# Kernel tuning notes

Hardware: AMD Instinct MI355X
Metric: run time of the kernel (lower is better)

The kernel has to match this reference:

```python
import jax, jax.numpy as jnp
import numpy as np

B, C, T, H, NCLS = 512, 22, 1000, 64, 4


def setup_inputs() -> dict:
    key = jax.random.key(0)
    ks = jax.random.split(key, 8)
    s_ih = 1.0 / np.sqrt(H)
    x = jax.random.normal(ks[0], (B, C, T), dtype=jnp.float32)
    # PyTorch LSTM params: gate order [i, f, g, o], each of size H
    W_ih = jax.random.uniform(ks[1], (4 * H, C), minval=-s_ih, maxval=s_ih, dtype=jnp.float32)
    W_hh = jax.random.uniform(ks[2], (4 * H, H), minval=-s_ih, maxval=s_ih, dtype=jnp.float32)
    b_ih = jax.random.uniform(ks[3], (4 * H,), minval=-s_ih, maxval=s_ih, dtype=jnp.float32)
    b_hh = jax.random.uniform(ks[4], (4 * H,), minval=-s_ih, maxval=s_ih, dtype=jnp.float32)
    s_fc = 1.0 / np.sqrt(H * T)
    W_fc = jax.random.uniform(ks[5], (NCLS, H * T), minval=-s_fc, maxval=s_fc, dtype=jnp.float32)
    b_fc = jax.random.uniform(ks[6], (NCLS,), minval=-s_fc, maxval=s_fc, dtype=jnp.float32)
    return {"x": x, "W_ih": W_ih, "W_hh": W_hh, "b_ih": b_ih, "b_hh": b_hh,
            "W_fc": W_fc, "b_fc": b_fc}


def _lstm(xs, W_ih, W_hh, b_ih, b_hh):
    # xs: [B, T, C] -> outputs [B, T, H]
    b = xs.shape[0]
    # precompute input projections for all timesteps: [T, B, 4H]
    x_proj = jnp.einsum('btc,gc->tbg', xs, W_ih) + (b_ih + b_hh)
    h0 = jnp.zeros((b, W_hh.shape[1]), xs.dtype)
    c0 = jnp.zeros_like(h0)

    def step(carry, xp):
        h, c = carry
        gates = xp + h @ W_hh.T  # [B, 4H]
        i, f, g, o = jnp.split(gates, 4, axis=-1)
        i = jax.nn.sigmoid(i)
        f = jax.nn.sigmoid(f)
        g = jnp.tanh(g)
        o = jax.nn.sigmoid(o)
        c = f * c + i * g
        h = o * jnp.tanh(c)
        return (h, c), h

    _, hs = jax.lax.scan(step, (h0, c0), x_proj)  # hs: [T, B, H]
    return jnp.transpose(hs, (1, 0, 2))  # [B, T, H]


def reference(x, W_ih, W_hh, b_ih, b_hh, W_fc, b_fc):
    xs = jnp.transpose(x, (0, 2, 1))  # [B, T, C]  (permute(0,2,1))
    hs = _lstm(xs, W_ih, W_hh, b_ih, b_hh)  # [B, T, H]
    flat = hs.reshape(hs.shape[0], -1)  # [B, T*H], time-major per row
    logits = flat @ W_fc.T + b_fc  # [B, 4]
    return jax.nn.softmax(logits, axis=1)
```

## Files before the change

kernel.cpp:

```cpp
#include <hip/hip_runtime.h>

#define BB   512
#define CC   22
#define TT   1000
#define HH   64
#define NCLS 4
#define TC   250
#define NCHUNK (TT / TC)
#define XROW 12

typedef _Float16 f16;
typedef __attribute__((ext_vector_type(2))) _Float16 h2;

__device__ __forceinline__ float sigm(float x) {
    return 1.0f / (1.0f + __expf(-x));
}
__device__ __forceinline__ float tanh_(float x) {
    float e = __expf(-2.0f * fabsf(x));
    float r = (1.0f - e) / (1.0f + e);
    return copysignf(r, x);
}

__device__ __forceinline__ h2 u2h(unsigned u) {
    union { unsigned u; h2 h; } c; c.u = u; return c.h;
}
__device__ __forceinline__ unsigned h2u(h2 h) {
    union { unsigned u; h2 h; } c; c.h = h; return c.u;
}

__global__ __launch_bounds__(64, 1) void lstm_wave(
    const float* __restrict__ x,
    const float* __restrict__ W_ih,
    const float* __restrict__ W_hh,
    const float* __restrict__ b_ih,
    const float* __restrict__ b_hh,
    const float* __restrict__ W_fc,
    const float* __restrict__ b_fc,
    float* __restrict__ out)
{
    __shared__ __align__(16) h2  xs[TC][XROW];
    __shared__ __align__(16) f16 hbuf[HH];

    const int lane = threadIdx.x;
    const int r    = blockIdx.x;

    unsigned whh[4][32];
    unsigned wih[4][11];
    float bias[4];
    #pragma unroll
    for (int g = 0; g < 4; ++g) {
        const int row = g * HH + lane;
        const float* wr = W_hh + row * HH;
        #pragma unroll
        for (int k = 0; k < 32; ++k)
            whh[g][k] = h2u(h2{(f16)wr[2 * k], (f16)wr[2 * k + 1]});
        const float* wi = W_ih + row * CC;
        #pragma unroll
        for (int k = 0; k < 11; ++k)
            wih[g][k] = h2u(h2{(f16)wi[2 * k], (f16)wi[2 * k + 1]});
        bias[g] = b_ih[row] + b_hh[row];
    }
    #pragma unroll
    for (int g = 0; g < 4; ++g) {
        #pragma unroll
        for (int k = 0; k < 32; ++k) asm volatile("" : "+v"(whh[g][k]));
        #pragma unroll
        for (int k = 0; k < 11; ++k) asm volatile("" : "+v"(wih[g][k]));
        asm volatile("" : "+v"(bias[g]));
    }

    hbuf[lane] = (f16)0.0f;
    float c = 0.0f;
    float fc0 = 0.f, fc1 = 0.f, fc2 = 0.f, fc3 = 0.f;
    const float* p0 = W_fc + 0 * (TT * HH) + lane;
    const float* p1 = W_fc + 1 * (TT * HH) + lane;
    const float* p2 = W_fc + 2 * (TT * HH) + lane;
    const float* p3 = W_fc + 3 * (TT * HH) + lane;
    const float* xrow = x + (size_t)r * (CC * TT);

    for (int chunk = 0; chunk < NCHUNK; ++chunk) {
        for (int tb = 0; tb < TC; tb += 64) {
            const int t = tb + lane;
            if (t < TC) {
                const float* gx = xrow + chunk * TC + t;
                union { h2 h[XROW]; uint4 q[3]; } U;
                #pragma unroll
                for (int k = 0; k < 11; ++k)
                    U.h[k] = h2{(f16)gx[(2 * k) * TT], (f16)gx[(2 * k + 1) * TT]};
                U.h[11] = h2{(f16)0.0f, (f16)0.0f};
                uint4* dst = (uint4*)&xs[t][0];
                dst[0] = U.q[0]; dst[1] = U.q[1]; dst[2] = U.q[2];
            }
        }

        for (int tt = 0; tt < TC; ++tt) {
            union { uint4 q[8]; h2 h[32]; } H;
            const uint4* hr = (const uint4*)hbuf;
            #pragma unroll
            for (int i = 0; i < 8; ++i) H.q[i] = hr[i];

            union { uint4 q[3]; h2 h[XROW]; } X;
            const uint4* xr = (const uint4*)&xs[tt][0];
            X.q[0] = xr[0]; X.q[1] = xr[1]; X.q[2] = xr[2];

            float w0 = *p0, w1 = *p1, w2 = *p2, w3 = *p3;
            p0 += HH; p1 += HH; p2 += HH; p3 += HH;

            float a0 = bias[0], a1 = bias[1], a2 = bias[2], a3 = bias[3];
            #pragma unroll
            for (int k = 0; k < 11; ++k) {
                a0 = __builtin_amdgcn_fdot2(X.h[k], u2h(wih[0][k]), a0, false);
                a1 = __builtin_amdgcn_fdot2(X.h[k], u2h(wih[1][k]), a1, false);
                a2 = __builtin_amdgcn_fdot2(X.h[k], u2h(wih[2][k]), a2, false);
                a3 = __builtin_amdgcn_fdot2(X.h[k], u2h(wih[3][k]), a3, false);
            }
            #pragma unroll
            for (int k = 0; k < 32; ++k) {
                a0 = __builtin_amdgcn_fdot2(H.h[k], u2h(whh[0][k]), a0, false);
                a1 = __builtin_amdgcn_fdot2(H.h[k], u2h(whh[1][k]), a1, false);
                a2 = __builtin_amdgcn_fdot2(H.h[k], u2h(whh[2][k]), a2, false);
                a3 = __builtin_amdgcn_fdot2(H.h[k], u2h(whh[3][k]), a3, false);
            }

            float iv = sigm(a0), fv = sigm(a1), gv = tanh_(a2), ov = sigm(a3);
            c = fv * c + iv * gv;
            float h = ov * tanh_(c);

            fc0 += h * w0; fc1 += h * w1; fc2 += h * w2; fc3 += h * w3;

            hbuf[lane] = (f16)h;
        }
    }

    #pragma unroll
    for (int off = 32; off; off >>= 1) {
        fc0 += __shfl_down(fc0, off);
        fc1 += __shfl_down(fc1, off);
        fc2 += __shfl_down(fc2, off);
        fc3 += __shfl_down(fc3, off);
    }
    if (lane == 0) {
        float l0 = fc0 + b_fc[0], l1 = fc1 + b_fc[1];
        float l2 = fc2 + b_fc[2], l3 = fc3 + b_fc[3];
        float m  = fmaxf(fmaxf(l0, l1), fmaxf(l2, l3));
        float e0 = __expf(l0 - m), e1 = __expf(l1 - m);
        float e2 = __expf(l2 - m), e3 = __expf(l3 - m);
        float s  = e0 + e1 + e2 + e3;
        float4 o; o.x = e0 / s; o.y = e1 / s; o.z = e2 / s; o.w = e3 / s;
        *(float4*)(out + r * NCLS) = o;
    }
}

extern "C" void kernel_launch(void* const* d_in, const int* in_sizes, int n_in,
                              void* d_out, int out_size, void* d_ws, size_t ws_size,
                              hipStream_t stream) {
    const float* x    = (const float*)d_in[0];
    const float* W_ih = (const float*)d_in[1];
    const float* W_hh = (const float*)d_in[2];
    const float* b_ih = (const float*)d_in[3];
    const float* b_hh = (const float*)d_in[4];
    const float* W_fc = (const float*)d_in[5];
    const float* b_fc = (const float*)d_in[6];
    float* out = (float*)d_out;

    lstm_wave<<<BB, 64, 0, stream>>>(x, W_ih, W_hh, b_ih, b_hh, W_fc, b_fc, out);
}
```

Measured before the change: 681.1 us.

## Precompute input projections per chunk with MFMA and defer FC accumulation

The input projection (W_ih·x) moves out of the serial recurrence. For each 64-step chunk it is computed with 16x16x32 f16 MFMA instructions and stored as packed f16 gate preactivations in shared memory. Hidden states of a chunk are kept in LDS, and the FC dot products run after the chunk, so the W_fc loads leave the critical serial path. Divisions are replaced by hardware reciprocals. The cost is extra LDS use, f16 rounding of the projected inputs, and W_ih fragments reloaded from global memory every chunk.

Result: slower. 1.281 ms (+88.1%).

```diff
diff --git a/kernel.cpp b/kernel.cpp
--- a/kernel.cpp
+++ b/kernel.cpp
@@ -5,30 +5,40 @@
 #define TT   1000
 #define HH   64
 #define NCLS 4
-#define TC   250
-#define NCHUNK (TT / TC)
-#define XROW 12
+#define FCW  (TT * HH)
+#define CH   64
+#define NCH  16
+#define XPS  528
 
 typedef _Float16 f16;
 typedef __attribute__((ext_vector_type(2))) _Float16 h2;
+typedef __attribute__((ext_vector_type(8))) _Float16 f16x8;
+typedef __attribute__((ext_vector_type(4))) float    f32x4;
+
+union U16x8 { uint4 q; f16x8 h; f16 e[8]; };
 
 __device__ __forceinline__ float sigm(float x) {
-    return 1.0f / (1.0f + __expf(-x));
+    float e = __expf(-x);
+    return __builtin_amdgcn_rcpf(1.0f + e);
 }
 __device__ __forceinline__ float tanh_(float x) {
     float e = __expf(-2.0f * fabsf(x));
-    float r = (1.0f - e) / (1.0f + e);
+    float r = (1.0f - e) * __builtin_amdgcn_rcpf(1.0f + e);
     return copysignf(r, x);
 }
-
 __device__ __forceinline__ h2 u2h(unsigned u) {
     union { unsigned u; h2 h; } c; c.u = u; return c.h;
 }
 __device__ __forceinline__ unsigned h2u(h2 h) {
     union { unsigned u; h2 h; } c; c.h = h; return c.u;
 }
-
-__global__ __launch_bounds__(64, 1) void lstm_wave(
+__device__ __forceinline__ unsigned pack2(float a, float b) {
+    union { unsigned u; h2 h; } c;
+    c.h = h2{(f16)a, (f16)b};
+    return c.u;
+}
+
+__global__ __launch_bounds__(64, 1) void lstm_fused(
     const float* __restrict__ x,
     const float* __restrict__ W_ih,
     const float* __restrict__ W_hh,
@@ -38,14 +48,16 @@
     const float* __restrict__ b_fc,
     float* __restrict__ out)
 {
-    __shared__ __align__(16) h2  xs[TC][XROW];
-    __shared__ __align__(16) f16 hbuf[HH];
+    __shared__ __align__(16) f16  xs[CH][32];
+    __shared__ __align__(16) char xpb[CH * XPS];
+    __shared__ __align__(16) f16  hst[CH][HH];
 
     const int lane = threadIdx.x;
     const int r    = blockIdx.x;
+    const int q    = lane >> 4;
+    const int c    = lane & 15;
 
     unsigned whh[4][32];
-    unsigned wih[4][11];
     float bias[4];
     #pragma unroll
     for (int g = 0; g < 4; ++g) {
@@ -53,82 +65,129 @@
         const float* wr = W_hh + row * HH;
         #pragma unroll
         for (int k = 0; k < 32; ++k)
-            whh[g][k] = h2u(h2{(f16)wr[2 * k], (f16)wr[2 * k + 1]});
-        const float* wi = W_ih + row * CC;
-        #pragma unroll
-        for (int k = 0; k < 11; ++k)
-            wih[g][k] = h2u(h2{(f16)wi[2 * k], (f16)wi[2 * k + 1]});
+            whh[g][k] = pack2(wr[2 * k], wr[2 * k + 1]);
         bias[g] = b_ih[row] + b_hh[row];
     }
     #pragma unroll
     for (int g = 0; g < 4; ++g) {
         #pragma unroll
         for (int k = 0; k < 32; ++k) asm volatile("" : "+v"(whh[g][k]));
-        #pragma unroll
-        for (int k = 0; k < 11; ++k) asm volatile("" : "+v"(wih[g][k]));
         asm volatile("" : "+v"(bias[g]));
     }
 
-    hbuf[lane] = (f16)0.0f;
-    float c = 0.0f;
+    hst[CH - 1][lane] = (f16)0.0f;
+    float cst = 0.0f;
     float fc0 = 0.f, fc1 = 0.f, fc2 = 0.f, fc3 = 0.f;
-    const float* p0 = W_fc + 0 * (TT * HH) + lane;
-    const float* p1 = W_fc + 1 * (TT * HH) + lane;
-    const float* p2 = W_fc + 2 * (TT * HH) + lane;
-    const float* p3 = W_fc + 3 * (TT * HH) + lane;
     const float* xrow = x + (size_t)r * (CC * TT);
 
-    for (int chunk = 0; chunk < NCHUNK; ++chunk) {
-        for (int tb = 0; tb < TC; tb += 64) {
-            const int t = tb + lane;
-            if (t < TC) {
-                const float* gx = xrow + chunk * TC + t;
-                union { h2 h[XROW]; uint4 q[3]; } U;
+    for (int ch = 0; ch < NCH; ++ch) {
+        const int T0 = ch * CH;
+        const int Lc = (T0 + CH <= TT) ? CH : (TT - T0);
+
+        {
+            const int t = lane;
+            union { h2 h[16]; uint4 qq[4]; } U;
+            if (t < Lc) {
+                const float* gx = xrow + T0 + t;
                 #pragma unroll
                 for (int k = 0; k < 11; ++k)
                     U.h[k] = h2{(f16)gx[(2 * k) * TT], (f16)gx[(2 * k + 1) * TT]};
-                U.h[11] = h2{(f16)0.0f, (f16)0.0f};
-                uint4* dst = (uint4*)&xs[t][0];
-                dst[0] = U.q[0]; dst[1] = U.q[1]; dst[2] = U.q[2];
-            }
-        }
-
-        for (int tt = 0; tt < TC; ++tt) {
-            union { uint4 q[8]; h2 h[32]; } H;
-            const uint4* hr = (const uint4*)hbuf;
+                #pragma unroll
+                for (int k = 11; k < 16; ++k) U.h[k] = h2{(f16)0.0f, (f16)0.0f};
+            } else {
+                #pragma unroll
+                for (int k = 0; k < 16; ++k) U.h[k] = h2{(f16)0.0f, (f16)0.0f};
+            }
+            uint4* dst = (uint4*)&xs[t][0];
+            dst[0] = U.qq[0]; dst[1] = U.qq[1]; dst[2] = U.qq[2]; dst[3] = U.qq[3];
+        }
+
+        #pragma unroll
+        for (int mt = 0; mt < 4; ++mt) {
+            f16x8 Afr[4];
             #pragma unroll
-            for (int i = 0; i < 8; ++i) H.q[i] = hr[i];
-
-            union { uint4 q[3]; h2 h[XROW]; } X;
-            const uint4* xr = (const uint4*)&xs[tt][0];
-            X.q[0] = xr[0]; X.q[1] = xr[1]; X.q[2] = xr[2];
-
-            float w0 = *p0, w1 = *p1, w2 = *p2, w3 = *p3;
-            p0 += HH; p1 += HH; p2 += HH; p3 += HH;
-
-            float a0 = bias[0], a1 = bias[1], a2 = bias[2], a3 = bias[3];
+            for (int g = 0; g < 4; ++g) {
+                const float* wbase = W_ih + (size_t)(g * HH + 16 * mt + c) * CC;
+                U16x8 u;
+                #pragma unroll
+                for (int e = 0; e < 8; ++e) {
+                    const int chn = 8 * q + e;
+                    u.e[e] = (f16)(chn < CC ? wbase[chn] : 0.0f);
+                }
+                Afr[g] = u.h;
+            }
             #pragma unroll
-            for (int k = 0; k < 11; ++k) {
-                a0 = __builtin_amdgcn_fdot2(X.h[k], u2h(wih[0][k]), a0, false);
-                a1 = __builtin_amdgcn_fdot2(X.h[k], u2h(wih[1][k]), a1, false);
-                a2 = __builtin_amdgcn_fdot2(X.h[k], u2h(wih[2][k]), a2, false);
-                a3 = __builtin_amdgcn_fdot2(X.h[k], u2h(wih[3][k]), a3, false);
-            }
-            #pragma unroll
-            for (int k = 0; k < 32; ++k) {
-                a0 = __builtin_amdgcn_fdot2(H.h[k], u2h(whh[0][k]), a0, false);
-                a1 = __builtin_amdgcn_fdot2(H.h[k], u2h(whh[1][k]), a1, false);
-                a2 = __builtin_amdgcn_fdot2(H.h[k], u2h(whh[2][k]), a2, false);
-                a3 = __builtin_amdgcn_fdot2(H.h[k], u2h(whh[3][k]), a3, false);
-            }
-
-            float iv = sigm(a0), fv = sigm(a1), gv = tanh_(a2), ov = sigm(a3);
-            c = fv * c + iv * gv;
-            float h = ov * tanh_(c);
-
-            fc0 += h * w0; fc1 += h * w1; fc2 += h * w2; fc3 += h * w3;
-
-            hbuf[lane] = (f16)h;
+            for (int tg = 0; tg < 4; ++tg) {
+                U16x8 Bf;
+                Bf.q = *(const uint4*)&xs[16 * tg + c][8 * q];
+                const f32x4 z = {0.f, 0.f, 0.f, 0.f};
+                f32x4 Di = __builtin_amdgcn_mfma_f32_16x16x32_f16(Afr[0], Bf.h, z, 0, 0, 0);
+                f32x4 Df = __builtin_amdgcn_mfma_f32_16x16x32_f16(Afr[1], Bf.h, z, 0, 0, 0);
+                f32x4 Dg = __builtin_amdgcn_mfma_f32_16x16x32_f16(Afr[2], Bf.h, z, 0, 0, 0);
+                f32x4 Do = __builtin_amdgcn_mfma_f32_16x16x32_f16(Afr[3], Bf.h, z, 0, 0, 0);
+                char* wp = xpb + (size_t)(16 * tg + c) * XPS + (16 * mt + 4 * q) * 8;
+                #pragma unroll
+                for (int rr = 0; rr < 4; ++rr) {
+                    uint2 v;
+                    v.x = pack2(Di[rr], Df[rr]);
+                    v.y = pack2(Dg[rr], Do[rr]);
+                    *(uint2*)(wp + rr * 8) = v;
+                }
+            }
+        }
+
+        for (int tt = 0; tt < Lc; ++tt) {
+            const int pr = (tt == 0) ? (CH - 1) : tt - 1;
+
+            const uint2 xv = *(const uint2*)(xpb + (size_t)tt * XPS + lane * 8);
+            const h2 pif = u2h(xv.x), pgo = u2h(xv.y);
+            float a0 = bias[0] + (float)pif[0];
+            float a1 = bias[1] + (float)pif[1];
+            float a2 = bias[2] + (float)pgo[0];
+            float a3 = bias[3] + (float)pgo[1];
+
+            const uint4* hr = (const uint4*)&hst[pr][0];
+            {
+                union { uint4 qq[4]; h2 h[16]; } H;
+                H.qq[0] = hr[0]; H.qq[1] = hr[1]; H.qq[2] = hr[2]; H.qq[3] = hr[3];
+                #pragma unroll
+                for (int k = 0; k < 16; ++k) {
+                    a0 = __builtin_amdgcn_fdot2(H.h[k], u2h(whh[0][k]), a0, false);
+                    a1 = __builtin_amdgcn_fdot2(H.h[k], u2h(whh[1][k]), a1, false);
+                    a2 = __builtin_amdgcn_fdot2(H.h[k], u2h(whh[2][k]), a2, false);
+                    a3 = __builtin_amdgcn_fdot2(H.h[k], u2h(whh[3][k]), a3, false);
+                }
+            }
+            {
+                union { uint4 qq[4]; h2 h[16]; } H;
+                H.qq[0] = hr[4]; H.qq[1] = hr[5]; H.qq[2] = hr[6]; H.qq[3] = hr[7];
+                #pragma unroll
+                for (int k = 0; k < 16; ++k) {
+                    a0 = __builtin_amdgcn_fdot2(H.h[k], u2h(whh[0][16 + k]), a0, false);
+                    a1 = __builtin_amdgcn_fdot2(H.h[k], u2h(whh[1][16 + k]), a1, false);
+                    a2 = __builtin_amdgcn_fdot2(H.h[k], u2h(whh[2][16 + k]), a2, false);
+                    a3 = __builtin_amdgcn_fdot2(H.h[k], u2h(whh[3][16 + k]), a3, false);
+                }
+            }
+
+            const float iv = sigm(a0), fv = sigm(a1);
+            const float gv = tanh_(a2), ov = sigm(a3);
+            cst = fv * cst + iv * gv;
+            const float h = ov * tanh_(cst);
+
+            hst[tt][lane] = (f16)h;
+        }
+
+        const float* w0 = W_fc + 0 * FCW + (size_t)T0 * HH + lane;
+        const float* w1 = W_fc + 1 * FCW + (size_t)T0 * HH + lane;
+        const float* w2 = W_fc + 2 * FCW + (size_t)T0 * HH + lane;
+        const float* w3 = W_fc + 3 * FCW + (size_t)T0 * HH + lane;
+        for (int tt = 0; tt < Lc; ++tt) {
+            const float hv = (float)hst[tt][lane];
+            fc0 += hv * w0[(size_t)tt * HH];
+            fc1 += hv * w1[(size_t)tt * HH];
+            fc2 += hv * w2[(size_t)tt * HH];
+            fc3 += hv * w3[(size_t)tt * HH];
         }
     }
 
@@ -140,13 +199,13 @@
         fc3 += __shfl_down(fc3, off);
     }
     if (lane == 0) {
-        float l0 = fc0 + b_fc[0], l1 = fc1 + b_fc[1];
-        float l2 = fc2 + b_fc[2], l3 = fc3 + b_fc[3];
-        float m  = fmaxf(fmaxf(l0, l1), fmaxf(l2, l3));
-        float e0 = __expf(l0 - m), e1 = __expf(l1 - m);
-        float e2 = __expf(l2 - m), e3 = __expf(l3 - m);
-        float s  = e0 + e1 + e2 + e3;
-        float4 o; o.x = e0 / s; o.y = e1 / s; o.z = e2 / s; o.w = e3 / s;
+        const float l0 = fc0 + b_fc[0], l1 = fc1 + b_fc[1];
+        const float l2 = fc2 + b_fc[2], l3 = fc3 + b_fc[3];
+        const float m  = fmaxf(fmaxf(l0, l1), fmaxf(l2, l3));
+        const float e0 = __expf(l0 - m), e1 = __expf(l1 - m);
+        const float e2 = __expf(l2 - m), e3 = __expf(l3 - m);
+        const float is = __builtin_amdgcn_rcpf(e0 + e1 + e2 + e3);
+        float4 o; o.x = e0 * is; o.y = e1 * is; o.z = e2 * is; o.w = e3 * is;
         *(float4*)(out + r * NCLS) = o;
     }
 }
@@ -163,5 +222,5 @@
     const float* b_fc = (const float*)d_in[6];
     float* out = (float*)d_out;
 
-    lstm_wave<<<BB, 64, 0, stream>>>(x, W_ih, W_hh, b_ih, b_hh, W_fc, b_fc, out);
-}
+    lstm_fused<<<BB, 64, 0, stream>>>(x, W_ih, W_hh, b_ih, b_hh, W_fc, b_fc, out);
+}
```

## Prefetch next-step input projection and defer FC accumulation to per-chunk pass

Applied to the files above, without the earlier changes.

Computes the input-projection dot products for timestep t+1 inside step t so they overlap the recurrent dot, shortening the serial dependency chain. Hidden states for each chunk are buffered in shared memory and the FC weights are consumed in a separate unrolled pass, removing global loads from the recurrence loop. Divisions in the activations and softmax are replaced with hardware reciprocal. This costs more shared memory and uses slightly less precise rcp math.

Measured after the change: 599.6 us. -12.0%, faster.

```diff
diff --git a/kernel.cpp b/kernel.cpp
--- a/kernel.cpp
+++ b/kernel.cpp
@@ -5,22 +5,22 @@
 #define TT   1000
 #define HH   64
 #define NCLS 4
-#define TC   250
-#define NCHUNK (TT / TC)
+#define FCW  (TT * HH)
+#define TCF  250
 #define XROW 12
 
 typedef _Float16 f16;
 typedef __attribute__((ext_vector_type(2))) _Float16 h2;
 
 __device__ __forceinline__ float sigm(float x) {
-    return 1.0f / (1.0f + __expf(-x));
+    float e = __expf(-x);
+    return __builtin_amdgcn_rcpf(1.0f + e);
 }
 __device__ __forceinline__ float tanh_(float x) {
     float e = __expf(-2.0f * fabsf(x));
-    float r = (1.0f - e) / (1.0f + e);
+    float r = (1.0f - e) * __builtin_amdgcn_rcpf(1.0f + e);
     return copysignf(r, x);
 }
-
 __device__ __forceinline__ h2 u2h(unsigned u) {
     union { unsigned u; h2 h; } c; c.u = u; return c.h;
 }
@@ -28,7 +28,21 @@
     union { unsigned u; h2 h; } c; c.h = h; return c.u;
 }
 
-__global__ __launch_bounds__(64, 1) void lstm_wave(
+#define XP_COMPUTE(TROW, O0, O1, O2, O3) do {                                  \
+    union { uint4 q[3]; h2 h[XROW]; } Xu_;                                     \
+    const uint4* xr_ = (const uint4*)&xs[(TROW)][0];                           \
+    Xu_.q[0] = xr_[0]; Xu_.q[1] = xr_[1]; Xu_.q[2] = xr_[2];                   \
+    O0 = bias[0]; O1 = bias[1]; O2 = bias[2]; O3 = bias[3];                    \
+    _Pragma("unroll")                                                          \
+    for (int k_ = 0; k_ < 11; ++k_) {                                          \
+        O0 = __builtin_amdgcn_fdot2(Xu_.h[k_], u2h(wih[0][k_]), O0, false);    \
+        O1 = __builtin_amdgcn_fdot2(Xu_.h[k_], u2h(wih[1][k_]), O1, false);    \
+        O2 = __builtin_amdgcn_fdot2(Xu_.h[k_], u2h(wih[2][k_]), O2, false);    \
+        O3 = __builtin_amdgcn_fdot2(Xu_.h[k_], u2h(wih[3][k_]), O3, false);    \
+    }                                                                          \
+} while (0)
+
+__global__ __launch_bounds__(64, 1) void lstm_one(
     const float* __restrict__ x,
     const float* __restrict__ W_ih,
     const float* __restrict__ W_hh,
@@ -38,15 +52,15 @@
     const float* __restrict__ b_fc,
     float* __restrict__ out)
 {
-    __shared__ __align__(16) h2  xs[TC][XROW];
-    __shared__ __align__(16) f16 hbuf[HH];
+    __shared__ __align__(16) h2  xs[TCF][XROW];
+    __shared__ __align__(16) f16 hst[TCF][HH];
 
     const int lane = threadIdx.x;
     const int r    = blockIdx.x;
 
     unsigned whh[4][32];
     unsigned wih[4][11];
-    float bias[4];
+    float    bias[4];
     #pragma unroll
     for (int g = 0; g < 4; ++g) {
         const int row = g * HH + lane;
@@ -69,20 +83,18 @@
         asm volatile("" : "+v"(bias[g]));
     }
 
-    hbuf[lane] = (f16)0.0f;
+    hst[TCF - 1][lane] = (f16)0.0f;
     float c = 0.0f;
     float fc0 = 0.f, fc1 = 0.f, fc2 = 0.f, fc3 = 0.f;
-    const float* p0 = W_fc + 0 * (TT * HH) + lane;
-    const float* p1 = W_fc + 1 * (TT * HH) + lane;
-    const float* p2 = W_fc + 2 * (TT * HH) + lane;
-    const float* p3 = W_fc + 3 * (TT * HH) + lane;
     const float* xrow = x + (size_t)r * (CC * TT);
 
-    for (int chunk = 0; chunk < NCHUNK; ++chunk) {
-        for (int tb = 0; tb < TC; tb += 64) {
+    for (int chunk = 0; chunk < 4; ++chunk) {
+        const int T0 = chunk * TCF;
+
+        for (int tb = 0; tb < TCF; tb += 64) {
             const int t = tb + lane;
-            if (t < TC) {
-                const float* gx = xrow + chunk * TC + t;
+            if (t < TCF) {
+                const float* gx = xrow + T0 + t;
                 union { h2 h[XROW]; uint4 q[3]; } U;
                 #pragma unroll
                 for (int k = 0; k < 11; ++k)
@@ -93,27 +105,25 @@
             }
         }
 
-        for (int tt = 0; tt < TC; ++tt) {
+        float xpc0, xpc1, xpc2, xpc3;
+        XP_COMPUTE(0, xpc0, xpc1, xpc2, xpc3);
+
+        for (int tt = 0; tt < TCF; ++tt) {
+            const int pr = (tt == 0) ? TCF - 1 : tt - 1;
+
             union { uint4 q[8]; h2 h[32]; } H;
-            const uint4* hr = (const uint4*)hbuf;
+            const uint4* hr = (const uint4*)&hst[pr][0];
             #pragma unroll
             for (int i = 0; i < 8; ++i) H.q[i] = hr[i];
 
-            union { uint4 q[3]; h2 h[XROW]; } X;
-            const uint4* xr = (const uint4*)&xs[tt][0];
-            X.q[0] = xr[0]; X.q[1] = xr[1]; X.q[2] = xr[2];
-
-            float w0 = *p0, w1 = *p1, w2 = *p2, w3 = *p3;
-            p0 += HH; p1 += HH; p2 += HH; p3 += HH;
-
-            float a0 = bias[0], a1 = bias[1], a2 = bias[2], a3 = bias[3];
-            #pragma unroll
-            for (int k = 0; k < 11; ++k) {
-                a0 = __builtin_amdgcn_fdot2(X.h[k], u2h(wih[0][k]), a0, false);
-                a1 = __builtin_amdgcn_fdot2(X.h[k], u2h(wih[1][k]), a1, false);
-                a2 = __builtin_amdgcn_fdot2(X.h[k], u2h(wih[2][k]), a2, false);
-                a3 = __builtin_amdgcn_fdot2(X.h[k], u2h(wih[3][k]), a3, false);
-            }
+            float xn0, xn1, xn2, xn3;
+            if (tt != TCF - 1) {
+                XP_COMPUTE(tt + 1, xn0, xn1, xn2, xn3);
+            } else {
+                xn0 = xn1 = xn2 = xn3 = 0.0f;
+            }
+
+            float a0 = xpc0, a1 = xpc1, a2 = xpc2, a3 = xpc3;
             #pragma unroll
             for (int k = 0; k < 32; ++k) {
                 a0 = __builtin_amdgcn_fdot2(H.h[k], u2h(whh[0][k]), a0, false);
@@ -122,13 +132,40 @@
                 a3 = __builtin_amdgcn_fdot2(H.h[k], u2h(whh[3][k]), a3, false);
             }
 
-            float iv = sigm(a0), fv = sigm(a1), gv = tanh_(a2), ov = sigm(a3);
+            const float iv = sigm(a0), fv = sigm(a1);
+            const float gv = tanh_(a2), ov = sigm(a3);
             c = fv * c + iv * gv;
-            float h = ov * tanh_(c);
-
-            fc0 += h * w0; fc1 += h * w1; fc2 += h * w2; fc3 += h * w3;
-
-            hbuf[lane] = (f16)h;
+            const float h = ov * tanh_(c);
+
+            hst[tt][lane] = (f16)h;
+
+            xpc0 = xn0; xpc1 = xn1; xpc2 = xn2; xpc3 = xn3;
+        }
+
+        const float* w0 = W_fc + 0 * FCW + (size_t)T0 * HH + lane;
+        const float* w1 = W_fc + 1 * FCW + (size_t)T0 * HH + lane;
+        const float* w2 = W_fc + 2 * FCW + (size_t)T0 * HH + lane;
+        const float* w3 = W_fc + 3 * FCW + (size_t)T0 * HH + lane;
+        for (int tb = 0; tb < TCF - 2; tb += 8) {
+            float wl0[8], wl1[8], wl2[8], wl3[8];
+            #pragma unroll
+            for (int u = 0; u < 8; ++u) {
+                const size_t o = (size_t)(tb + u) * HH;
+                wl0[u] = w0[o]; wl1[u] = w1[o]; wl2[u] = w2[o]; wl3[u] = w3[o];
+            }
+            #pragma unroll
+            for (int u = 0; u < 8; ++u) {
+                const float hv = (float)hst[tb + u][lane];
+                fc0 += hv * wl0[u]; fc1 += hv * wl1[u];
+                fc2 += hv * wl2[u]; fc3 += hv * wl3[u];
+            }
+        }
+        #pragma unroll
+        for (int tt = TCF - 2; tt < TCF; ++tt) {
+            const size_t o = (size_t)tt * HH;
+            const float hv = (float)hst[tt][lane];
+            fc0 += hv * w0[o]; fc1 += hv * w1[o];
+            fc2 += hv * w2[o]; fc3 += hv * w3[o];
         }
     }
 
@@ -140,13 +177,13 @@
         fc3 += __shfl_down(fc3, off);
     }
     if (lane == 0) {
-        float l0 = fc0 + b_fc[0], l1 = fc1 + b_fc[1];
-        float l2 = fc2 + b_fc[2], l3 = fc3 + b_fc[3];
-        float m  = fmaxf(fmaxf(l0, l1), fmaxf(l2, l3));
-        float e0 = __expf(l0 - m), e1 = __expf(l1 - m);
-        float e2 = __expf(l2 - m), e3 = __expf(l3 - m);
-        float s  = e0 + e1 + e2 + e3;
-        float4 o; o.x = e0 / s; o.y = e1 / s; o.z = e2 / s; o.w = e3 / s;
+        const float l0 = fc0 + b_fc[0], l1 = fc1 + b_fc[1];
+        const float l2 = fc2 + b_fc[2], l3 = fc3 + b_fc[3];
+        const float m  = fmaxf(fmaxf(l0, l1), fmaxf(l2, l3));
+        const float e0 = __expf(l0 - m), e1 = __expf(l1 - m);
+        const float e2 = __expf(l2 - m), e3 = __expf(l3 - m);
+        const float is = __builtin_amdgcn_rcpf(e0 + e1 + e2 + e3);
+        float4 o; o.x = e0 * is; o.y = e1 * is; o.z = e2 * is; o.w = e3 * is;
         *(float4*)(out + r * NCLS) = o;
     }
 }
@@ -163,5 +200,5 @@
     const float* b_fc = (const float*)d_in[6];
     float* out = (float*)d_out;
 
-    lstm_wave<<<BB, 64, 0, stream>>>(x, W_ih, W_hh, b_ih, b_hh, W_fc, b_fc, out);
-}
+    lstm_one<<<BB, 64, 0, stream>>>(x, W_ih, W_hh, b_ih, b_hh, W_fc, b_fc, out);
+}
```
